# Performance work log

Hardware: AMD Instinct MI355X
Metric: run time of the kernel (lower is better)

Reference implementation:

```python
import jax, jax.numpy as jnp
import numpy as np

B = 512            # molecules
M = 24             # atoms per molecule
N = B * M          # total nodes
F = 128            # num_features
NRBF = 20          # num_rbf_features
CUTOFF = 5.0       # cutoff_dist
NUM_ATOM_TYPES = 100


def setup_inputs() -> dict:
    key = jax.random.key(0)
    ks = jax.random.split(key, 8)
    atoms = jax.random.randint(ks[0], (N,), 0, NUM_ATOM_TYPES, dtype=jnp.int64 if jax.config.jax_enable_x64 else jnp.int32)
    # positions in a ~6A box per molecule so many pairs fall under the 5A cutoff
    atom_positions = jax.random.uniform(ks[1], (N, 3), dtype=jnp.float32) * 6.0
    graph_indexes = jnp.repeat(jnp.arange(B), M)
    emb = jax.random.normal(ks[2], (NUM_ATOM_TYPES, F), dtype=jnp.float32)
    W1 = jax.random.normal(ks[3], (F, F), dtype=jnp.float32) / np.sqrt(F)
    b1 = jnp.zeros((F,), dtype=jnp.float32)
    W2 = jax.random.normal(ks[4], (F, 3 * F), dtype=jnp.float32) / np.sqrt(F)
    b2 = jnp.zeros((3 * F,), dtype=jnp.float32)
    Wf = jax.random.normal(ks[5], (NRBF, 3 * F), dtype=jnp.float32) / np.sqrt(NRBF)
    bf = jnp.zeros((3 * F,), dtype=jnp.float32)
    return {"atoms": atoms, "atom_positions": atom_positions, "graph_indexes": graph_indexes,
            "emb": emb, "W1": W1, "b1": b1, "W2": W2, "b2": b2, "Wf": Wf, "bf": bf}


def _painn_forward(atoms, atom_positions, emb, W1, b1, W2, b2, Wf, bf):
    # node embeddings s_i^0 and zero vector features v_i^0
    s = emb[atoms].reshape(B, M, F)                       # [B,M,F]
    v = jnp.zeros((B, M, F, 3), dtype=s.dtype)            # [B,M,F,3]
    pos = atom_positions.reshape(B, M, 3)

    # per-molecule dense neighbor list (same-molecule pairs within cutoff)
    r = pos[:, :, None, :] - pos[:, None, :, :]           # r_ij = pos_i - pos_j  [B,M,M,3]
    d = jnp.linalg.norm(r, axis=-1)                       # [B,M,M]
    mask = (d < CUTOFF) & ~jnp.eye(M, dtype=bool)         # exclude self (d=0 -> RBF div-by-zero)
    d_safe = jnp.where(mask, d, 1.0)

    # RBF: sin(n*pi*d/cutoff)/d, n = 1..20
    n = jnp.arange(1, NRBF + 1, dtype=s.dtype)
    rbf = jnp.sin(n * (jnp.pi / CUTOFF) * d_safe[..., None]) / d_safe[..., None]   # [B,M,M,20]
    Wedge = rbf @ Wf + bf                                 # edge filter  [B,M,M,3F]

    # node MLP phi(s_j): Linear(F,F) -> SiLU -> Linear(F,3F)
    phi = jax.nn.silu(s @ W1 + b1) @ W2 + b2              # [B,M,3F]

    # gather phi over j, modulate by edge filter, mask invalid edges
    msg = Wedge * phi[:, None, :, :] * mask[..., None]    # [B,M,M,3F]
    ds_m, dv_v, dv_r = jnp.split(msg, 3, axis=-1)         # each [B,M,M,F]

    ds = ds_m.sum(axis=2)                                 # scatter-sum over neighbors j -> [B,M,F]
    rhat = r / d_safe[..., None]                          # unit directions
    dv = (jnp.einsum('bijf,bjfc->bifc', dv_v, v)
          + jnp.einsum('bijf,bijc->bifc', dv_r, rhat))    # [B,M,F,3]

    s_new = s + ds
    v_new = v + dv
    return jnp.concatenate([s_new, v_new.reshape(B, M, 3 * F)], axis=-1)  # [B,M,4F]


def reference(atoms, atom_positions, graph_indexes, emb, W1, b1, W2, b2, Wf, bf):
    del graph_indexes  # batch structure is encoded by the fixed [B,M] layout
    return _painn_forward(atoms, atom_positions, emb, W1, b1, W2, b2, Wf, bf)
```

## Files before the change

kernel.cpp:

```cpp
#include <hip/hip_runtime.h>
#include <hip/hip_bf16.h>
#include <hip/hip_fp16.h>
#include <math.h>

#define B 512
#define M 24
#define F 128
#define NRBF 20
#define CUTOFF 5.0f
#define SA_LD 44
#define SH_LD 140
#define CHUNK 8


typedef __attribute__((ext_vector_type(8))) short short8;
typedef __attribute__((ext_vector_type(4))) float f32x4;

#define KIDX(g, e) ((((e) >> 2) << 4) + 4 * (g) + ((e) & 3))

__device__ __forceinline__ unsigned f2bf(float x) {
    unsigned u = __builtin_bit_cast(unsigned, x);
    return (u + 0x7FFFu + ((u >> 16) & 1u)) >> 16;
}
__device__ __forceinline__ unsigned f2h(float x) {
    return (unsigned)__builtin_bit_cast(unsigned short, __float2half(x));
}

__device__ __forceinline__ short8 pack_frag(unsigned u0, unsigned u1,
                                            unsigned u2, unsigned u3) {
    uint4 t = make_uint4(u0, u1, u2, u3);
    return __builtin_bit_cast(short8, t);
}

__device__ __forceinline__ short8 load_wfrag(const float* __restrict__ W, int ld,
                                             int col, int kbase, int g) {
    unsigned u[4];
#pragma unroll
    for (int q = 0; q < 4; ++q) {
        int k0 = kbase + KIDX(g, 2 * q);
        int k1 = kbase + KIDX(g, 2 * q + 1);
        u[q] = f2bf(W[(size_t)k0 * ld + col]) | (f2bf(W[(size_t)k1 * ld + col]) << 16);
    }
    return pack_frag(u[0], u[1], u[2], u[3]);
}

__device__ __forceinline__ short8 load_wffrag(const float* __restrict__ Wf,
                                              const float* __restrict__ bfv,
                                              int col, int g) {
    unsigned u[4];
#pragma unroll
    for (int q = 0; q < 4; ++q) {
        int k0 = KIDX(g, 2 * q);
        int k1 = KIDX(g, 2 * q + 1);
        float f0 = (k0 < NRBF) ? Wf[(size_t)k0 * (3 * F) + col] : (k0 == NRBF ? bfv[col] : 0.f);
        float f1 = (k1 < NRBF) ? Wf[(size_t)k1 * (3 * F) + col] : (k1 == NRBF ? bfv[col] : 0.f);
        u[q] = f2bf(f0) | (f2bf(f1) << 16);
    }
    return pack_frag(u[0], u[1], u[2], u[3]);
}

__device__ __forceinline__ short8 load_afrag(const short* sp, int row, int ldsh,
                                             int kbase, int g) {
    const short* p = sp + row * ldsh + kbase + 4 * g;
    uint2 lo = *(const uint2*)(p);
    uint2 hi = *(const uint2*)(p + 16);
    uint4 t = make_uint4(lo.x, lo.y, hi.x, hi.y);
    return __builtin_bit_cast(short8, t);
}

__global__ __launch_bounds__(512, 2) void painn_kernel(
    const int* __restrict__ atoms,
    const float* __restrict__ apos,
    const float* __restrict__ emb,
    const float* __restrict__ W1, const float* __restrict__ b1,
    const float* __restrict__ W2, const float* __restrict__ b2,
    const float* __restrict__ Wf, const float* __restrict__ bf,
    float* __restrict__ out)
{
    __shared__ __attribute__((aligned(16))) short sH[32 * SH_LD];
    __shared__ __attribute__((aligned(16))) short sA[2][CHUNK * 32 * SA_LD];
    __shared__ __attribute__((aligned(16))) unsigned sGeoH[2][CHUNK * 32 * 2];
    __shared__ __attribute__((aligned(16))) float sPos[M][4];

    const int tid  = threadIdx.x;
    const int b    = blockIdx.x;
    const int wid  = tid >> 6;
    const int lane = tid & 63;
    const int g    = lane >> 4;
    const int lrow = lane & 15;
    const int f2   = wid * 16 + lrow;

    const float kth = 3.14159265358979323846f / CUTOFF;

    for (int idx = tid; idx < M * 32; idx += 512) {
        int node = idx >> 5;
        int f4 = idx & 31;
        int a = atoms[b * M + node];
        float4 v = reinterpret_cast<const float4*>(emb + (size_t)a * F)[f4];
        unsigned u0 = f2bf(v.x) | (f2bf(v.y) << 16);
        unsigned u1 = f2bf(v.z) | (f2bf(v.w) << 16);
        *reinterpret_cast<uint2*>(&sH[node * SH_LD + f4 * 4]) = make_uint2(u0, u1);
    }
    for (int t = tid; t < 560; t += 512)
        reinterpret_cast<unsigned*>(sH)[1680 + t] = 0u;
    if (tid < M * 3) sPos[tid / 3][tid % 3] = apos[(size_t)b * M * 3 + tid];
    __syncthreads();

    {
        float b1v = b1[f2];
        f32x4 c[2] = {{0.f, 0.f, 0.f, 0.f}, {0.f, 0.f, 0.f, 0.f}};
#pragma unroll
        for (int ks = 0; ks < 4; ++ks) {
            short8 bfrag = load_wfrag(W1, F, f2, ks * 32, g);
            short8 a0 = load_afrag(sH, lrow, SH_LD, ks * 32, g);
            short8 a1 = load_afrag(sH, 16 + lrow, SH_LD, ks * 32, g);
            c[0] = __builtin_amdgcn_mfma_f32_16x16x32_bf16(a0, bfrag, c[0], 0, 0, 0);
            c[1] = __builtin_amdgcn_mfma_f32_16x16x32_bf16(a1, bfrag, c[1], 0, 0, 0);
        }
        __syncthreads();
#pragma unroll
        for (int rt = 0; rt < 2; ++rt)
#pragma unroll
            for (int r = 0; r < 4; ++r) {
                int row = rt * 16 + g * 4 + r;
                float x = c[rt][r] + b1v;
                float h = x / (1.0f + __expf(-x));
                sH[row * SH_LD + f2] = (short)f2bf(h);
            }
    }
    __syncthreads();

    float ph0[8], ph2[8];
#pragma unroll
    for (int half = 0; half < 2; ++half) {
        int wcol = half ? (256 + f2) : f2;
        float b2v = b2[wcol];
        f32x4 c[2] = {{0.f, 0.f, 0.f, 0.f}, {0.f, 0.f, 0.f, 0.f}};
#pragma unroll
        for (int ks = 0; ks < 4; ++ks) {
            short8 bfrag = load_wfrag(W2, 3 * F, wcol, ks * 32, g);
            short8 a0 = load_afrag(sH, lrow, SH_LD, ks * 32, g);
            short8 a1 = load_afrag(sH, 16 + lrow, SH_LD, ks * 32, g);
            c[0] = __builtin_amdgcn_mfma_f32_16x16x32_bf16(a0, bfrag, c[0], 0, 0, 0);
            c[1] = __builtin_amdgcn_mfma_f32_16x16x32_bf16(a1, bfrag, c[1], 0, 0, 0);
        }
#pragma unroll
        for (int rt = 0; rt < 2; ++rt)
#pragma unroll
            for (int r = 0; r < 4; ++r) {
                if (half == 0) ph0[rt * 4 + r] = c[rt][r] + b2v;
                else           ph2[rt * 4 + r] = c[rt][r] + b2v;
            }
    }

    short8 wfrag0 = load_wffrag(Wf, bf, f2, g);
    short8 wfrag2 = load_wffrag(Wf, bf, 256 + f2, g);

    const int pil = tid >> 5;
    const int pj  = tid & 31;

    unsigned pk[16];
    unsigned gxy, gz;

    auto produce = [&](int ic) {
#pragma unroll
        for (int q = 0; q < 16; ++q) pk[q] = 0u;
        gxy = 0u; gz = 0u;
        int i = ic * CHUNK + pil;
        if (pj < M && pj != i) {
            float dx = sPos[i][0] - sPos[pj][0];
            float dy = sPos[i][1] - sPos[pj][1];
            float dz = sPos[i][2] - sPos[pj][2];
            float d = sqrtf(dx * dx + dy * dy + dz * dz);
            if (d < CUTOFF) {
                float inv = 1.0f / d;
                float s1, c1;
                __sincosf(kth * d, &s1, &c1);
                float cc = 2.0f * c1;
                float vp = s1 * inv;
                float vc = 2.0f * s1 * c1 * inv;
                pk[0] = f2bf(vp) | (f2bf(vc) << 16);
#pragma unroll
                for (int q = 1; q < 10; ++q) {
                    float v3 = cc * vc - vp;
                    float v4 = cc * v3 - vc;
                    pk[q] = f2bf(v3) | (f2bf(v4) << 16);
                    vp = v3; vc = v4;
                }
                pk[10] = 0x3F80u;
                gxy = f2h(dx * inv) | (f2h(dy * inv) << 16);
                gz  = f2h(dz * inv);
            }
        }
    };
    auto writebuf = [&](int buf) {
        short* rp = &sA[buf][(pil * 32 + pj) * SA_LD];
#pragma unroll
        for (int q = 0; q < 8; ++q)
            *reinterpret_cast<uint2*>(rp + q * 4) = make_uint2(pk[2 * q], pk[2 * q + 1]);
        *reinterpret_cast<uint2*>(&sGeoH[buf][(pil * 32 + pj) * 2]) = make_uint2(gxy, gz);
    };

    if (tid < 256) { produce(0); writebuf(0); }
    __syncthreads();

    for (int ic = 0; ic < 3; ++ic) {
        const int buf = ic & 1;
        if (ic < 2 && tid < 256) { produce(ic + 1); writebuf(buf ^ 1); }
#pragma unroll 2
        for (int il = 0; il < CHUNK; ++il) {
            const int i = ic * CHUNK + il;
            float s0 = 0.f, ax = 0.f, ay = 0.f, az = 0.f;
#pragma unroll
            for (int rt = 0; rt < 2; ++rt) {
                short8 afr = load_afrag(&sA[buf][0], il * 32 + rt * 16 + lrow, SA_LD, 0, g);
                f32x4 z4 = {0.f, 0.f, 0.f, 0.f};
                f32x4 c0 = __builtin_amdgcn_mfma_f32_16x16x32_bf16(afr, wfrag0, z4, 0, 0, 0);
                f32x4 c2 = __builtin_amdgcn_mfma_f32_16x16x32_bf16(afr, wfrag2, z4, 0, 0, 0);
#pragma unroll
                for (int r = 0; r < 4; ++r) {
                    int j = rt * 16 + g * 4 + r;
                    uint2 gw = *reinterpret_cast<const uint2*>(&sGeoH[buf][(il * 32 + j) * 2]);
                    __half2 hxy = __builtin_bit_cast(__half2, gw.x);
                    float gx = __low2float(hxy);
                    float gy = __high2float(hxy);
                    float gzf = __low2float(__builtin_bit_cast(__half2, gw.y));
                    s0 = fmaf(c0[r], ph0[rt * 4 + r], s0);
                    float m2 = c2[r] * ph2[rt * 4 + r];
                    ax = fmaf(m2, gx, ax);
                    ay = fmaf(m2, gy, ay);
                    az = fmaf(m2, gzf, az);
                }
            }
            s0 += __shfl_xor(s0, 32);
            ax += __shfl_xor(ax, 32);
            ay += __shfl_xor(ay, 32);
            az += __shfl_xor(az, 32);
            float keep = (g == 0) ? s0 : (g == 1) ? ax : (g == 2) ? ay : az;
            float send = (g == 0) ? ax : (g == 1) ? s0 : (g == 2) ? az : ay;
            float v = keep + __shfl_xor(send, 16);
            const int node = b * M + i;
            float outv = v;
            int col;
            if (g == 0) {
                outv += emb[(size_t)atoms[node] * F + f2];
                col = f2;
            } else {
                col = F + 3 * f2 + (g - 1);
            }
            out[(size_t)node * (4 * F) + col] = outv;
        }
        __syncthreads();
    }
}

extern "C" void kernel_launch(void* const* d_in, const int* in_sizes, int n_in,
                              void* d_out, int out_size, void* d_ws, size_t ws_size,
                              hipStream_t stream) {
    const int*   atoms = (const int*)d_in[0];
    const float* apos  = (const float*)d_in[1];
    const float* emb = (const float*)d_in[3];
    const float* W1  = (const float*)d_in[4];
    const float* b1  = (const float*)d_in[5];
    const float* W2  = (const float*)d_in[6];
    const float* b2  = (const float*)d_in[7];
    const float* Wf  = (const float*)d_in[8];
    const float* bf  = (const float*)d_in[9];
    float* out = (float*)d_out;

    painn_kernel<<<B, 512, 0, stream>>>(atoms, apos, emb, W1, b1, W2, b2, Wf, bf, out);
}
```

Baseline: 31.02 us.

## Reorder edge tiles so each lane group owns one atom, drop shuffle reductions

Edge rows in shared memory are permuted so that in each 16-row MFMA tile every lane group g handles a different target atom i. Each lane can then accumulate its atom's sums fully across 8 tiles without cross-lane shuffle reductions, and writes all four outputs directly. Phi values are packed as bf16 pairs through a new shared buffer and held in 32 registers per lane, and geometry is read with wider vector loads from a padded layout. The cost is more register pressure (php[32]), bf16 rounding of phi, and less evenly spread output stores.

```diff
diff --git a/kernel.cpp b/kernel.cpp
--- a/kernel.cpp
+++ b/kernel.cpp
@@ -10,6 +10,7 @@
 #define CUTOFF 5.0f
 #define SA_LD 44
 #define SH_LD 140
+#define GEO_LD 34
 #define CHUNK 8
 
 
@@ -79,7 +80,8 @@
 {
     __shared__ __attribute__((aligned(16))) short sH[32 * SH_LD];
     __shared__ __attribute__((aligned(16))) short sA[2][CHUNK * 32 * SA_LD];
-    __shared__ __attribute__((aligned(16))) unsigned sGeoH[2][CHUNK * 32 * 2];
+    __shared__ __attribute__((aligned(16))) unsigned sGeoH[2][CHUNK * GEO_LD * 2];
+    __shared__ __attribute__((aligned(16))) unsigned sPhiP[32 * F];
     __shared__ __attribute__((aligned(16))) float sPos[M][4];
 
     const int tid  = threadIdx.x;
@@ -130,26 +132,35 @@
     }
     __syncthreads();
 
-    float ph0[8], ph2[8];
-#pragma unroll
-    for (int half = 0; half < 2; ++half) {
-        int wcol = half ? (256 + f2) : f2;
-        float b2v = b2[wcol];
-        f32x4 c[2] = {{0.f, 0.f, 0.f, 0.f}, {0.f, 0.f, 0.f, 0.f}};
-#pragma unroll
-        for (int ks = 0; ks < 4; ++ks) {
-            short8 bfrag = load_wfrag(W2, 3 * F, wcol, ks * 32, g);
-            short8 a0 = load_afrag(sH, lrow, SH_LD, ks * 32, g);
-            short8 a1 = load_afrag(sH, 16 + lrow, SH_LD, ks * 32, g);
-            c[0] = __builtin_amdgcn_mfma_f32_16x16x32_bf16(a0, bfrag, c[0], 0, 0, 0);
-            c[1] = __builtin_amdgcn_mfma_f32_16x16x32_bf16(a1, bfrag, c[1], 0, 0, 0);
+    {
+        float ph0v[8], ph2v[8];
+#pragma unroll
+        for (int half = 0; half < 2; ++half) {
+            int wcol = half ? (256 + f2) : f2;
+            float b2v = b2[wcol];
+            f32x4 c[2] = {{0.f, 0.f, 0.f, 0.f}, {0.f, 0.f, 0.f, 0.f}};
+#pragma unroll
+            for (int ks = 0; ks < 4; ++ks) {
+                short8 bfrag = load_wfrag(W2, 3 * F, wcol, ks * 32, g);
+                short8 a0 = load_afrag(sH, lrow, SH_LD, ks * 32, g);
+                short8 a1 = load_afrag(sH, 16 + lrow, SH_LD, ks * 32, g);
+                c[0] = __builtin_amdgcn_mfma_f32_16x16x32_bf16(a0, bfrag, c[0], 0, 0, 0);
+                c[1] = __builtin_amdgcn_mfma_f32_16x16x32_bf16(a1, bfrag, c[1], 0, 0, 0);
+            }
+#pragma unroll
+            for (int rt = 0; rt < 2; ++rt)
+#pragma unroll
+                for (int r = 0; r < 4; ++r) {
+                    if (half == 0) ph0v[rt * 4 + r] = c[rt][r] + b2v;
+                    else           ph2v[rt * 4 + r] = c[rt][r] + b2v;
+                }
         }
 #pragma unroll
         for (int rt = 0; rt < 2; ++rt)
 #pragma unroll
             for (int r = 0; r < 4; ++r) {
-                if (half == 0) ph0[rt * 4 + r] = c[rt][r] + b2v;
-                else           ph2[rt * 4 + r] = c[rt][r] + b2v;
+                int row = rt * 16 + g * 4 + r;
+                sPhiP[row * F + f2] = f2bf(ph0v[rt * 4 + r]) | (f2bf(ph2v[rt * 4 + r]) << 16);
             }
     }
 
@@ -194,61 +205,62 @@
         }
     };
     auto writebuf = [&](int buf) {
-        short* rp = &sA[buf][(pil * 32 + pj) * SA_LD];
+        int arow = (pil >> 2) * 128 + (pj >> 2) * 16 + (pil & 3) * 4 + (pj & 3);
+        short* rp = &sA[buf][arow * SA_LD];
 #pragma unroll
         for (int q = 0; q < 8; ++q)
             *reinterpret_cast<uint2*>(rp + q * 4) = make_uint2(pk[2 * q], pk[2 * q + 1]);
-        *reinterpret_cast<uint2*>(&sGeoH[buf][(pil * 32 + pj) * 2]) = make_uint2(gxy, gz);
+        *reinterpret_cast<uint2*>(&sGeoH[buf][(pil * GEO_LD + pj) * 2]) = make_uint2(gxy, gz);
     };
 
     if (tid < 256) { produce(0); writebuf(0); }
     __syncthreads();
+
+    unsigned php[32];
+#pragma unroll
+    for (int j = 0; j < 32; ++j) php[j] = sPhiP[j * F + f2];
 
     for (int ic = 0; ic < 3; ++ic) {
         const int buf = ic & 1;
         if (ic < 2 && tid < 256) { produce(ic + 1); writebuf(buf ^ 1); }
-#pragma unroll 2
-        for (int il = 0; il < CHUNK; ++il) {
-            const int i = ic * CHUNK + il;
+#pragma unroll
+        for (int bb = 0; bb < 2; ++bb) {
+            const int iloc = bb * 4 + g;
+            const int i = ic * CHUNK + iloc;
             float s0 = 0.f, ax = 0.f, ay = 0.f, az = 0.f;
 #pragma unroll
-            for (int rt = 0; rt < 2; ++rt) {
-                short8 afr = load_afrag(&sA[buf][0], il * 32 + rt * 16 + lrow, SA_LD, 0, g);
+            for (int mm = 0; mm < 8; ++mm) {
+                short8 afr = load_afrag(&sA[buf][0], bb * 128 + mm * 16 + lrow, SA_LD, 0, g);
                 f32x4 z4 = {0.f, 0.f, 0.f, 0.f};
                 f32x4 c0 = __builtin_amdgcn_mfma_f32_16x16x32_bf16(afr, wfrag0, z4, 0, 0, 0);
                 f32x4 c2 = __builtin_amdgcn_mfma_f32_16x16x32_bf16(afr, wfrag2, z4, 0, 0, 0);
+                const uint4* gp = reinterpret_cast<const uint4*>(
+                    &sGeoH[buf][(iloc * GEO_LD + mm * 4) * 2]);
+                uint4 ga = gp[0], gb = gp[1];
 #pragma unroll
                 for (int r = 0; r < 4; ++r) {
-                    int j = rt * 16 + g * 4 + r;
-                    uint2 gw = *reinterpret_cast<const uint2*>(&sGeoH[buf][(il * 32 + j) * 2]);
-                    __half2 hxy = __builtin_bit_cast(__half2, gw.x);
+                    unsigned pxy = (r == 0) ? ga.x : (r == 1) ? ga.z : (r == 2) ? gb.x : gb.z;
+                    unsigned pzz = (r == 0) ? ga.y : (r == 1) ? ga.w : (r == 2) ? gb.y : gb.w;
+                    __half2 hxy = __builtin_bit_cast(__half2, pxy);
                     float gx = __low2float(hxy);
                     float gy = __high2float(hxy);
-                    float gzf = __low2float(__builtin_bit_cast(__half2, gw.y));
-                    s0 = fmaf(c0[r], ph0[rt * 4 + r], s0);
-                    float m2 = c2[r] * ph2[rt * 4 + r];
+                    float gzf = __low2float(__builtin_bit_cast(__half2, pzz));
+                    unsigned pp = php[mm * 4 + r];
+                    float p0 = __builtin_bit_cast(float, pp << 16);
+                    float p2 = __builtin_bit_cast(float, pp & 0xFFFF0000u);
+                    s0 = fmaf(c0[r], p0, s0);
+                    float m2 = c2[r] * p2;
                     ax = fmaf(m2, gx, ax);
                     ay = fmaf(m2, gy, ay);
                     az = fmaf(m2, gzf, az);
                 }
             }
-            s0 += __shfl_xor(s0, 32);
-            ax += __shfl_xor(ax, 32);
-            ay += __shfl_xor(ay, 32);
-            az += __shfl_xor(az, 32);
-            float keep = (g == 0) ? s0 : (g == 1) ? ax : (g == 2) ? ay : az;
-            float send = (g == 0) ? ax : (g == 1) ? s0 : (g == 2) ? az : ay;
-            float v = keep + __shfl_xor(send, 16);
             const int node = b * M + i;
-            float outv = v;
-            int col;
-            if (g == 0) {
-                outv += emb[(size_t)atoms[node] * F + f2];
-                col = f2;
-            } else {
-                col = F + 3 * f2 + (g - 1);
-            }
-            out[(size_t)node * (4 * F) + col] = outv;
+            float* o = out + (size_t)node * (4 * F);
+            o[f2] = emb[(size_t)atoms[node] * F + f2] + s0;
+            o[F + 3 * f2 + 0] = ax;
+            o[F + 3 * f2 + 1] = ay;
+            o[F + 3 * f2 + 2] = az;
         }
         __syncthreads();
     }
```

Result: slower. 34.50 us (+11.2%).
